# Performance work log

Hardware: AMD Instinct MI355X
Metric: run time of the kernel (lower is better)

## Reference

```python
import jax, jax.numpy as jnp
import numpy as np

N = 100000
E = 1600000
IN_DIM, HID, OUT = 512, 128, 16


def setup_inputs() -> dict:
    key = jax.random.key(0)
    ks = jax.random.split(key, 8)
    x = jax.random.normal(ks[0], (N, IN_DIM), dtype=jnp.float32)
    edge_index = jax.random.randint(ks[1], (2, E), 0, N, dtype=jnp.int64)
    # GCNConv params (Glorot-ish scale) and Linear head
    W1 = jax.random.normal(ks[2], (IN_DIM, HID), dtype=jnp.float32) / np.sqrt(IN_DIM)
    b1 = jnp.zeros((HID,), dtype=jnp.float32)
    W2 = jax.random.normal(ks[3], (HID, HID), dtype=jnp.float32) / np.sqrt(HID)
    b2 = jnp.zeros((HID,), dtype=jnp.float32)
    Wl = jax.random.normal(ks[4], (HID, OUT), dtype=jnp.float32) / np.sqrt(HID)
    bl = jnp.zeros((OUT,), dtype=jnp.float32)
    return {"x": x, "edge_index": edge_index, "W1": W1, "b1": b1,
            "W2": W2, "b2": b2, "Wl": Wl, "bl": bl}


def _gcn_conv(x, W, b, src, dst, deg_inv_sqrt, deg_inv):
    # h = x @ W ; out[dst] += norm * h[src]; self-loop adds h[i]/deg[i]
    h = x @ W                                           # [N, D]
    norm = deg_inv_sqrt[src] * deg_inv_sqrt[dst]        # [E]
    msgs = h[src] * norm[:, None]                       # [E, D] gather
    agg = jax.ops.segment_sum(msgs, dst, num_segments=x.shape[0])  # scatter
    agg = agg + h * deg_inv[:, None]                    # self-loop term
    return agg + b


def reference(x, edge_index, W1, b1, W2, b2, Wl, bl):
    src, dst = edge_index[0], edge_index[1]
    n = x.shape[0]
    ones = jnp.ones(src.shape[0], dtype=x.dtype)
    # degree with self-loops (PyG gcn_norm counts in-degree at target + 1)
    deg = jax.ops.segment_sum(ones, dst, num_segments=n) + 1.0
    deg_inv_sqrt = jax.lax.rsqrt(deg)
    deg_inv = 1.0 / deg

    h = _gcn_conv(x, W1, b1, src, dst, deg_inv_sqrt, deg_inv)
    h = jax.nn.relu(h)
    # dropout: inference mode (training=False) -> identity
    h = _gcn_conv(h, W2, b2, src, dst, deg_inv_sqrt, deg_inv)
    embeddings = jax.nn.relu(h)
    out = embeddings @ Wl + bl
    return out, embeddings
```

## Files before the change

### kernel.cpp

```cpp
#include <hip/hip_runtime.h>

#define NN 100000
#define EE 1600000
#define IND 512
#define HIDD 128
#define OUTD 16
#define GEMM_BLKS 782

typedef __bf16 bf16x8 __attribute__((ext_vector_type(8)));
typedef float f32x4 __attribute__((ext_vector_type(4)));

__device__ __forceinline__ ushort f2bf(float f) {
    union { float f; uint u; } v; v.f = f;
    uint r = v.u + 0x7FFFu + ((v.u >> 16) & 1u);
    return (ushort)(r >> 16);
}

__device__ __forceinline__ uint pk2bf(float a, float b) {
    __bf16 x = (__bf16)a, y = (__bf16)b;
    ushort ux = *(ushort*)&x, uy = *(ushort*)&y;
    return (uint)ux | ((uint)uy << 16);
}

__global__ void k_prep(const float* __restrict__ W1, const float* __restrict__ W2,
                       ushort* __restrict__ Wt1, ushort* __restrict__ Wt2) {
    int b = blockIdx.x, tid = threadIdx.x;
    if (b < 256) {
        int i = b * 256 + tid;
        int k = i >> 7, n = i & 127;
        Wt1[n * 512 + k] = f2bf(W1[i]);
    } else {
        int i = (b - 256) * 256 + tid;
        int k = i >> 7, n = i & 127;
        Wt2[n * 128 + k] = f2bf(W2[i]);
    }
}

__global__ void k_scan_local(const int* __restrict__ deg, int* __restrict__ incl,
                             int* __restrict__ bsum) {
    __shared__ int s[256];
    int tid = threadIdx.x;
    int i = blockIdx.x * 256 + tid;
    int v = (i < NN) ? deg[i] : 0;
    s[tid] = v;
    __syncthreads();
    for (int off = 1; off < 256; off <<= 1) {
        int t = (tid >= off) ? s[tid - off] : 0;
        __syncthreads();
        s[tid] += t;
        __syncthreads();
    }
    if (i < NN) incl[i] = s[tid];
    if (tid == 255) bsum[blockIdx.x] = s[255];
}

__global__ void k_scan_bsum(const int* __restrict__ bsum, int* __restrict__ boff, int n) {
    __shared__ int s[512];
    int tid = threadIdx.x;
    int v = (tid < n) ? bsum[tid] : 0;
    s[tid] = v;
    __syncthreads();
    for (int off = 1; off < 512; off <<= 1) {
        int t = (tid >= off) ? s[tid - off] : 0;
        __syncthreads();
        s[tid] += t;
        __syncthreads();
    }
    if (tid < n) boff[tid] = s[tid] - v;
}

__global__ void k_scan_final(const int* __restrict__ incl, const int* __restrict__ deg,
                             const int* __restrict__ boff, int* __restrict__ rs,
                             float* __restrict__ dis, float* __restrict__ dinv) {
    int i = blockIdx.x * 256 + threadIdx.x;
    if (i < NN) {
        int d = deg[i];
        int v = incl[i] + boff[i >> 8];
        rs[i] = v - d;
        if (i == NN - 1) rs[NN] = v;
        float df = (float)(d + 1);
        dis[i] = rsqrtf(df);
        dinv[i] = 1.0f / df;
    }
}

__global__ void k_fill(const int* __restrict__ src, const int* __restrict__ dst,
                       const int* __restrict__ pos, const int* __restrict__ rs,
                       const float* __restrict__ dis, int2* __restrict__ ew) {
    int i = blockIdx.x * blockDim.x + threadIdx.x;
    int stride = gridDim.x * blockDim.x;
    for (; i < EE; i += stride) {
        int d = dst[i];
        int s = src[i];
        ew[rs[d] + pos[i]] = make_int2(s, __float_as_int(dis[s] * dis[d]));
    }
}

template <int K, bool AFP32>
__device__ __forceinline__ void gemm_ldsw(const void* __restrict__ Ap,
                                          const ushort* __restrict__ Wt,
                                          ushort* __restrict__ C, int blk) {
    constexpr int KH = (K > 256) ? 256 : K;
    constexpr int HALVES = K / KH;
    constexpr int CH = KH / 8;
    constexpr int ROWB = CH * 16;
    constexpr int NTh = KH / 32;
    __shared__ char Wl_s[128 * ROWB];

    int tid = threadIdx.x;
    int row0 = blk * 128;
    int wid = tid >> 6, lane = tid & 63;
    int lm = lane & 15, lkq = lane >> 4;
    int m = row0 + wid * 16 + lm;
    int mc = (m < NN) ? m : NN - 1;

    const float* Arow32 = (const float*)Ap + (size_t)mc * K;
    const ushort* Arow16 = (const ushort*)Ap + (size_t)mc * K;

    f32x4 acc[8];
#pragma unroll
    for (int q = 0; q < 8; q++) acc[q] = (f32x4){0.f, 0.f, 0.f, 0.f};

#pragma unroll
    for (int h = 0; h < HALVES; h++) {
        int kh = h * KH;
        if (h > 0) __syncthreads();
        {
            int n = tid >> 2, qt = tid & 3;
            const ushort* wsrc = Wt + (size_t)n * K + kh + qt * (KH / 4);
#pragma unroll
            for (int j = 0; j < CH / 4; j++) {
                int c = qt * (CH / 4) + j;
                uint4 v = *(const uint4*)(wsrc + j * 8);
                int cs = c ^ (n & 7);
                *(uint4*)(Wl_s + n * ROWB + cs * 16) = v;
            }
        }
        __syncthreads();

        float4 pa32[4][2];
        uint4 pa16[4];
#pragma unroll
        for (int p = 0; p < 4 && p < NTh; p++) {
            if (AFP32) {
                const float* pp = Arow32 + kh + p * 32 + lkq * 8;
                pa32[p][0] = *(const float4*)pp;
                pa32[p][1] = *(const float4*)(pp + 4);
            } else {
                pa16[p] = *(const uint4*)(Arow16 + kh + p * 32 + lkq * 8);
            }
        }
#pragma unroll
        for (int t = 0; t < NTh; t++) {
            constexpr int PM = 3;
            bf16x8 xf;
            if (AFP32) {
                uint4 u;
                u.x = pk2bf(pa32[t & PM][0].x, pa32[t & PM][0].y);
                u.y = pk2bf(pa32[t & PM][0].z, pa32[t & PM][0].w);
                u.z = pk2bf(pa32[t & PM][1].x, pa32[t & PM][1].y);
                u.w = pk2bf(pa32[t & PM][1].z, pa32[t & PM][1].w);
                xf = *(bf16x8*)&u;
            } else {
                xf = *(bf16x8*)&pa16[t & PM];
            }
            if (t + 4 < NTh) {
                if (AFP32) {
                    const float* pp = Arow32 + kh + (t + 4) * 32 + lkq * 8;
                    pa32[t & PM][0] = *(const float4*)pp;
                    pa32[t & PM][1] = *(const float4*)(pp + 4);
                } else {
                    pa16[t & PM] = *(const uint4*)(Arow16 + kh + (t + 4) * 32 + lkq * 8);
                }
            }
#pragma unroll
            for (int q = 0; q < 8; q++) {
                int n_ = q * 16 + lm;
                int c = t * 4 + lkq;
                uint4 w = *(const uint4*)(Wl_s + n_ * ROWB + ((c ^ (n_ & 7)) << 4));
                acc[q] = __builtin_amdgcn_mfma_f32_16x16x32_bf16(*(bf16x8*)&w, xf, acc[q], 0, 0, 0);
            }
        }
    }

    int cn4 = (lane >> 4) * 4;
    if (m < NN) {
#pragma unroll
        for (int q = 0; q < 8; q++) {
            int n = q * 16 + cn4;
            uint2 o;
            o.x = (uint)f2bf(acc[q][0]) | ((uint)f2bf(acc[q][1]) << 16);
            o.y = (uint)f2bf(acc[q][2]) | ((uint)f2bf(acc[q][3]) << 16);
            *(uint2*)(C + (size_t)m * 128 + n) = o;
        }
    }
}

__global__ __launch_bounds__(512, 4) void k_mega1(const float* __restrict__ x,
                                                  const ushort* __restrict__ Wt1,
                                                  ushort* __restrict__ C,
                                                  const int* __restrict__ dst,
                                                  int* __restrict__ deg,
                                                  int* __restrict__ pos) {
    gemm_ldsw<IND, true>(x, Wt1, C, blockIdx.x);
    int base = blockIdx.x * 2048;
#pragma unroll
    for (int j = 0; j < 4; j++) {
        int i = base + j * 512 + threadIdx.x;
        if (i < EE) pos[i] = atomicAdd(&deg[dst[i]], 1);
    }
}

__global__ __launch_bounds__(512, 4) void k_gemm2(const ushort* __restrict__ A,
                                                  const ushort* __restrict__ Wt,
                                                  ushort* __restrict__ C) {
    gemm_ldsw<HIDD, false>(A, Wt, C, blockIdx.x);
}

template <bool OUTF32>
__global__ __launch_bounds__(256) void k_agg(const ushort* __restrict__ h,
                                             const int* __restrict__ rs,
                                             const int2* __restrict__ ew,
                                             const float* __restrict__ dinv,
                                             const float* __restrict__ bias,
                                             void* __restrict__ yv) {
    int node = blockIdx.x * 4 + (threadIdx.x >> 6);
    int lane = threadIdx.x & 63;
    if (node >= NN) return;
    int half = lane >> 5, c = lane & 31;
    const uint2* h64 = (const uint2*)h;

    float acc0 = 0.f, acc1 = 0.f, acc2 = 0.f, acc3 = 0.f;
    if (half == 0) {
        float dv = dinv[node];
        uint2 sv = h64[(size_t)node * 32 + c];
        acc0 = __uint_as_float(sv.x << 16) * dv;
        acc1 = __uint_as_float(sv.x & 0xffff0000u) * dv;
        acc2 = __uint_as_float(sv.y << 16) * dv;
        acc3 = __uint_as_float(sv.y & 0xffff0000u) * dv;
    }

    int e = rs[node], e1 = rs[node + 1];

#define EL(i) int2 p##i = ew[e + 2 * i + half]; \
              uint2 g##i = h64[(size_t)(uint)p##i.x * 32 + c];
#define EA(i) { float w##i = __int_as_float(p##i.y); \
    acc0 += w##i * __uint_as_float(g##i.x << 16); \
    acc1 += w##i * __uint_as_float(g##i.x & 0xffff0000u); \
    acc2 += w##i * __uint_as_float(g##i.y << 16); \
    acc3 += w##i * __uint_as_float(g##i.y & 0xffff0000u); }

    for (; e + 16 <= e1; e += 16) {
        EL(0) EL(1) EL(2) EL(3) EL(4) EL(5) EL(6) EL(7)
        EA(0) EA(1) EA(2) EA(3) EA(4) EA(5) EA(6) EA(7)
    }
    for (; e + 4 <= e1; e += 4) {
        EL(0) EL(1)
        EA(0) EA(1)
    }
    if (e + 2 <= e1) {
        EL(0)
        EA(0)
        e += 2;
    }
    if (e < e1 && half == 0) {
        int2 p = ew[e];
        uint2 g = h64[(size_t)(uint)p.x * 32 + c];
        float w = __int_as_float(p.y);
        acc0 += w * __uint_as_float(g.x << 16);
        acc1 += w * __uint_as_float(g.x & 0xffff0000u);
        acc2 += w * __uint_as_float(g.y << 16);
        acc3 += w * __uint_as_float(g.y & 0xffff0000u);
    }
#undef EL
#undef EA

    acc0 += __shfl_xor(acc0, 32, 64);
    acc1 += __shfl_xor(acc1, 32, 64);
    acc2 += __shfl_xor(acc2, 32, 64);
    acc3 += __shfl_xor(acc3, 32, 64);

    if (half == 0) {
        float4 bv = *(const float4*)(bias + c * 4);
        acc0 = fmaxf(acc0 + bv.x, 0.f);
        acc1 = fmaxf(acc1 + bv.y, 0.f);
        acc2 = fmaxf(acc2 + bv.z, 0.f);
        acc3 = fmaxf(acc3 + bv.w, 0.f);
        if (OUTF32) {
            *(float4*)((float*)yv + (size_t)node * 128 + c * 4) =
                make_float4(acc0, acc1, acc2, acc3);
        } else {
            uint2 o;
            o.x = (uint)f2bf(acc0) | ((uint)f2bf(acc1) << 16);
            o.y = (uint)f2bf(acc2) | ((uint)f2bf(acc3) << 16);
            *(uint2*)((ushort*)yv + (size_t)node * 128 + c * 4) = o;
        }
    }
}

__global__ __launch_bounds__(256) void k_out(const float* __restrict__ emb,
                                             const float* __restrict__ Wl,
                                             const float* __restrict__ bl,
                                             float* __restrict__ out) {
    __shared__ float wl_s[128 * 16];
    __shared__ float es[16][129];
    int tid = threadIdx.x;
    int row0 = blockIdx.x * 16;
#pragma unroll
    for (int p = 0; p < 8; p++) wl_s[p * 256 + tid] = Wl[p * 256 + tid];
#pragma unroll
    for (int p = 0; p < 8; p++) {
        int idx = p * 256 + tid;
        int r = idx >> 7, c = idx & 127;
        int gr = row0 + r;
        es[r][c] = (gr < NN) ? emb[(size_t)gr * 128 + c] : 0.0f;
    }
    __syncthreads();
    int r = tid >> 4, o = tid & 15;
    float acc = bl[o];
#pragma unroll
    for (int k = 0; k < 128; k++) acc += es[r][k] * wl_s[k * 16 + o];
    int gr = row0 + r;
    if (gr < NN) out[(size_t)gr * 16 + o] = acc;
}

extern "C" void kernel_launch(void* const* d_in, const int* in_sizes, int n_in,
                              void* d_out, int out_size, void* d_ws, size_t ws_size,
                              hipStream_t stream) {
    const float* x  = (const float*)d_in[0];
    const int* ei   = (const int*)d_in[1];
    const float* W1 = (const float*)d_in[2];
    const float* b1 = (const float*)d_in[3];
    const float* W2 = (const float*)d_in[4];
    const float* b2 = (const float*)d_in[5];
    const float* Wl = (const float*)d_in[6];
    const float* bl = (const float*)d_in[7];
    const int* src = ei;
    const int* dst = ei + EE;

    float* outp = (float*)d_out;
    float* emb  = outp + (size_t)NN * OUTD;

    int2* ew    = (int2*)d_ws;
    int* pos    = (int*)(ew + EE);
    ushort* h_a = (ushort*)(pos + EE);
    ushort* h_b = h_a + (size_t)NN * 128;
    ushort* Wt1 = h_b + (size_t)NN * 128;
    ushort* Wt2 = Wt1 + 128 * 512;
    int* deg    = (int*)(Wt2 + 128 * 128);
    float* dis  = (float*)(deg + NN);
    float* dinv = dis + NN;
    int* incl   = (int*)(dinv + NN);
    int* rs     = incl + NN;
    int* bsum   = rs + NN + 8;
    int* boff   = bsum + 512;

    const int NB_N = (NN + 255) / 256;

    hipMemsetAsync(deg, 0, (size_t)NN * sizeof(int), stream);
    k_prep<<<320, 256, 0, stream>>>(W1, W2, Wt1, Wt2);
    k_mega1<<<GEMM_BLKS, 512, 0, stream>>>(x, Wt1, h_a, dst, deg, pos);
    k_scan_local<<<NB_N, 256, 0, stream>>>(deg, incl, bsum);
    k_scan_bsum<<<1, 512, 0, stream>>>(bsum, boff, NB_N);
    k_scan_final<<<NB_N, 256, 0, stream>>>(incl, deg, boff, rs, dis, dinv);
    k_fill<<<2048, 256, 0, stream>>>(src, dst, pos, rs, dis, ew);

    k_agg<false><<<(NN + 3) / 4, 256, 0, stream>>>(h_a, rs, ew, dinv, b1, h_b);
    k_gemm2<<<GEMM_BLKS, 512, 0, stream>>>(h_b, Wt2, h_a);
    k_agg<true><<<(NN + 3) / 4, 256, 0, stream>>>(h_a, rs, ew, dinv, b2, emb);
    k_out<<<(NN + 15) / 16, 256, 0, stream>>>(emb, Wl, bl, outp);
}
```

Before: 375.4 us.

## Split GEMMs into persistent K-pass kernels and separate degree counting

Replaces the one-tile-per-block GEMM with persistent kernels. Each block loads a K-slice of the weights into LDS once, then loops over 16-row tiles per wave. The 512-deep first GEMM becomes two passes over K halves, with an fp32 partial buffer (reusing emb) that the second pass adds before converting to bf16. The degree atomics move out of the fused GEMM into a separate kernel. The aim is to amortise weight loads and raise load-level parallelism, at the cost of an extra fp32 round-trip to global memory and one more launch.

```diff
diff --git a/kernel.cpp b/kernel.cpp
--- a/kernel.cpp
+++ b/kernel.cpp
@@ -5,7 +5,7 @@
 #define IND 512
 #define HIDD 128
 #define OUTD 16
-#define GEMM_BLKS 782
+#define NTILES 6250
 
 typedef __bf16 bf16x8 __attribute__((ext_vector_type(8)));
 typedef float f32x4 __attribute__((ext_vector_type(4)));
@@ -34,6 +34,13 @@
         int k = i >> 7, n = i & 127;
         Wt2[n * 128 + k] = f2bf(W2[i]);
     }
+}
+
+__global__ void k_deg(const int* __restrict__ dst, int* __restrict__ deg,
+                      int* __restrict__ pos) {
+    int i = blockIdx.x * blockDim.x + threadIdx.x;
+    int stride = gridDim.x * blockDim.x;
+    for (; i < EE; i += stride) pos[i] = atomicAdd(&deg[dst[i]], 1);
 }
 
 __global__ void k_scan_local(const int* __restrict__ deg, int* __restrict__ incl,
@@ -96,125 +103,105 @@
     }
 }
 
-template <int K, bool AFP32>
-__device__ __forceinline__ void gemm_ldsw(const void* __restrict__ Ap,
-                                          const ushort* __restrict__ Wt,
-                                          ushort* __restrict__ C, int blk) {
-    constexpr int KH = (K > 256) ? 256 : K;
-    constexpr int HALVES = K / KH;
+template <bool AFP32, int PASS>
+__global__ __launch_bounds__(256) void k_gemmp(const void* __restrict__ Ap, int Astride,
+                                               int koff,
+                                               const ushort* __restrict__ Wt, int Wstride,
+                                               float* __restrict__ hp,
+                                               ushort* __restrict__ hout,
+                                               int wstride_total) {
+    constexpr int KH = AFP32 ? 256 : 128;
     constexpr int CH = KH / 8;
-    constexpr int ROWB = CH * 16;
-    constexpr int NTh = KH / 32;
-    __shared__ char Wl_s[128 * ROWB];
+    constexpr int NSTEP = KH / 32;
+    __shared__ char Wl[128 * CH * 16];
 
     int tid = threadIdx.x;
-    int row0 = blk * 128;
     int wid = tid >> 6, lane = tid & 63;
     int lm = lane & 15, lkq = lane >> 4;
-    int m = row0 + wid * 16 + lm;
-    int mc = (m < NN) ? m : NN - 1;
-
-    const float* Arow32 = (const float*)Ap + (size_t)mc * K;
-    const ushort* Arow16 = (const ushort*)Ap + (size_t)mc * K;
-
-    f32x4 acc[8];
-#pragma unroll
-    for (int q = 0; q < 8; q++) acc[q] = (f32x4){0.f, 0.f, 0.f, 0.f};
-
-#pragma unroll
-    for (int h = 0; h < HALVES; h++) {
-        int kh = h * KH;
-        if (h > 0) __syncthreads();
-        {
-            int n = tid >> 2, qt = tid & 3;
-            const ushort* wsrc = Wt + (size_t)n * K + kh + qt * (KH / 4);
-#pragma unroll
-            for (int j = 0; j < CH / 4; j++) {
-                int c = qt * (CH / 4) + j;
-                uint4 v = *(const uint4*)(wsrc + j * 8);
-                int cs = c ^ (n & 7);
-                *(uint4*)(Wl_s + n * ROWB + cs * 16) = v;
+
+    {
+        int n = tid >> 1, q = tid & 1;
+        const ushort* wsrc = Wt + (size_t)n * Wstride + koff;
+#pragma unroll
+        for (int j = 0; j < CH / 2; j++) {
+            int c = q * (CH / 2) + j;
+            uint4 v = *(const uint4*)(wsrc + c * 8);
+            int cs = (c & ~7) | ((c ^ n) & 7);
+            *(uint4*)(Wl + n * (CH * 16) + cs * 16) = v;
+        }
+    }
+    __syncthreads();
+
+    const float* Af = (const float*)Ap;
+    const ushort* Ab = (const ushort*)Ap;
+
+    for (int t = blockIdx.x * 4 + wid; t < NTILES; t += wstride_total) {
+        int r = t * 16 + lm;
+
+        float4 pa32[8][2];
+        uint4 pa16[4];
+        if (AFP32) {
+            const float* ar = Af + (size_t)r * Astride + koff + lkq * 8;
+#pragma unroll
+            for (int p = 0; p < 8; p++) {
+                pa32[p][0] = *(const float4*)(ar + p * 32);
+                pa32[p][1] = *(const float4*)(ar + p * 32 + 4);
             }
-        }
-        __syncthreads();
-
-        float4 pa32[4][2];
-        uint4 pa16[4];
-#pragma unroll
-        for (int p = 0; p < 4 && p < NTh; p++) {
-            if (AFP32) {
-                const float* pp = Arow32 + kh + p * 32 + lkq * 8;
-                pa32[p][0] = *(const float4*)pp;
-                pa32[p][1] = *(const float4*)(pp + 4);
-            } else {
-                pa16[p] = *(const uint4*)(Arow16 + kh + p * 32 + lkq * 8);
-            }
-        }
-#pragma unroll
-        for (int t = 0; t < NTh; t++) {
-            constexpr int PM = 3;
+        } else {
+            const ushort* ar = Ab + (size_t)r * Astride + lkq * 8;
+#pragma unroll
+            for (int p = 0; p < 4; p++) pa16[p] = *(const uint4*)(ar + p * 32);
+        }
+
+        f32x4 acc[8];
+#pragma unroll
+        for (int q = 0; q < 8; q++) acc[q] = (f32x4){0.f, 0.f, 0.f, 0.f};
+
+#pragma unroll
+        for (int ts = 0; ts < NSTEP; ts++) {
             bf16x8 xf;
             if (AFP32) {
                 uint4 u;
-                u.x = pk2bf(pa32[t & PM][0].x, pa32[t & PM][0].y);
-                u.y = pk2bf(pa32[t & PM][0].z, pa32[t & PM][0].w);
-                u.z = pk2bf(pa32[t & PM][1].x, pa32[t & PM][1].y);
-                u.w = pk2bf(pa32[t & PM][1].z, pa32[t & PM][1].w);
+                u.x = pk2bf(pa32[ts][0].x, pa32[ts][0].y);
+                u.y = pk2bf(pa32[ts][0].z, pa32[ts][0].w);
+                u.z = pk2bf(pa32[ts][1].x, pa32[ts][1].y);
+                u.w = pk2bf(pa32[ts][1].z, pa32[ts][1].w);
                 xf = *(bf16x8*)&u;
             } else {
-                xf = *(bf16x8*)&pa16[t & PM];
-            }
-            if (t + 4 < NTh) {
-                if (AFP32) {
-                    const float* pp = Arow32 + kh + (t + 4) * 32 + lkq * 8;
-                    pa32[t & PM][0] = *(const float4*)pp;
-                    pa32[t & PM][1] = *(const float4*)(pp + 4);
-                } else {
-                    pa16[t & PM] = *(const uint4*)(Arow16 + kh + (t + 4) * 32 + lkq * 8);
-                }
+                xf = *(bf16x8*)&pa16[ts];
             }
 #pragma unroll
             for (int q = 0; q < 8; q++) {
                 int n_ = q * 16 + lm;
-                int c = t * 4 + lkq;
-                uint4 w = *(const uint4*)(Wl_s + n_ * ROWB + ((c ^ (n_ & 7)) << 4));
-                acc[q] = __builtin_amdgcn_mfma_f32_16x16x32_bf16(*(bf16x8*)&w, xf, acc[q], 0, 0, 0);
+                int c = ts * 4 + lkq;
+                int cs = (c & ~7) | ((c ^ n_) & 7);
+                bf16x8 wf = *(const bf16x8*)(Wl + n_ * (CH * 16) + cs * 16);
+                acc[q] = __builtin_amdgcn_mfma_f32_16x16x32_bf16(wf, xf, acc[q], 0, 0, 0);
             }
         }
-    }
-
-    int cn4 = (lane >> 4) * 4;
-    if (m < NN) {
+
+        int cn4 = lkq * 4;
+        size_t mrow = (size_t)r * 128;
 #pragma unroll
         for (int q = 0; q < 8; q++) {
             int n = q * 16 + cn4;
-            uint2 o;
-            o.x = (uint)f2bf(acc[q][0]) | ((uint)f2bf(acc[q][1]) << 16);
-            o.y = (uint)f2bf(acc[q][2]) | ((uint)f2bf(acc[q][3]) << 16);
-            *(uint2*)(C + (size_t)m * 128 + n) = o;
-        }
-    }
-}
-
-__global__ __launch_bounds__(512, 4) void k_mega1(const float* __restrict__ x,
-                                                  const ushort* __restrict__ Wt1,
-                                                  ushort* __restrict__ C,
-                                                  const int* __restrict__ dst,
-                                                  int* __restrict__ deg,
-                                                  int* __restrict__ pos) {
-    gemm_ldsw<IND, true>(x, Wt1, C, blockIdx.x);
-    int base = blockIdx.x * 2048;
-#pragma unroll
-    for (int j = 0; j < 4; j++) {
-        int i = base + j * 512 + threadIdx.x;
-        if (i < EE) pos[i] = atomicAdd(&deg[dst[i]], 1);
-    }
-}
-
-__global__ __launch_bounds__(512, 4) void k_gemm2(const ushort* __restrict__ A,
-                                                  const ushort* __restrict__ Wt,
-                                                  ushort* __restrict__ C) {
-    gemm_ldsw<HIDD, false>(A, Wt, C, blockIdx.x);
+            if (PASS == 0) {
+                *(f32x4*)(hp + mrow + n) = acc[q];
+            } else if (PASS == 1) {
+                f32x4 pv = *(const f32x4*)(hp + mrow + n);
+                f32x4 s = acc[q] + pv;
+                uint2 o;
+                o.x = pk2bf(s[0], s[1]);
+                o.y = pk2bf(s[2], s[3]);
+                *(uint2*)(hout + mrow + n) = o;
+            } else {
+                uint2 o;
+                o.x = pk2bf(acc[q][0], acc[q][1]);
+                o.y = pk2bf(acc[q][2], acc[q][3]);
+                *(uint2*)(hout + mrow + n) = o;
+            }
+        }
+    }
 }
 
 template <bool OUTF32>
@@ -359,14 +346,18 @@
 
     hipMemsetAsync(deg, 0, (size_t)NN * sizeof(int), stream);
     k_prep<<<320, 256, 0, stream>>>(W1, W2, Wt1, Wt2);
-    k_mega1<<<GEMM_BLKS, 512, 0, stream>>>(x, Wt1, h_a, dst, deg, pos);
+
+    k_gemmp<true, 0><<<512, 256, 0, stream>>>(x, IND, 0,   Wt1, 512, emb, nullptr, 2048);
+    k_gemmp<true, 1><<<512, 256, 0, stream>>>(x, IND, 256, Wt1, 512, emb, h_a,     2048);
+
+    k_deg<<<2048, 256, 0, stream>>>(dst, deg, pos);
     k_scan_local<<<NB_N, 256, 0, stream>>>(deg, incl, bsum);
     k_scan_bsum<<<1, 512, 0, stream>>>(bsum, boff, NB_N);
     k_scan_final<<<NB_N, 256, 0, stream>>>(incl, deg, boff, rs, dis, dinv);
     k_fill<<<2048, 256, 0, stream>>>(src, dst, pos, rs, dis, ew);
 
     k_agg<false><<<(NN + 3) / 4, 256, 0, stream>>>(h_a, rs, ew, dinv, b1, h_b);
-    k_gemm2<<<GEMM_BLKS, 512, 0, stream>>>(h_b, Wt2, h_a);
+    k_gemmp<false, 2><<<1024, 256, 0, stream>>>(h_b, HIDD, 0, Wt2, 128, nullptr, h_a, 4096);
     k_agg<true><<<(NN + 3) / 4, 256, 0, stream>>>(h_a, rs, ew, dinv, b2, emb);
     k_out<<<(NN + 15) / 16, 256, 0, stream>>>(emb, Wl, bl, outp);
 }
```

Result: slower. 453.7 us (+20.8%).
